# Optimization experiments

Measured on AMD Instinct MI355X. Metric: run time of the kernel, lower is better.

The kernel has to match this reference:

```python
import jax, jax.numpy as jnp
import numpy as np

N_HEAD = 16

def setup_inputs() -> dict:
    key = jax.random.key(0)
    k1, k2, k3 = jax.random.split(key, 3)
    B, T, C = 4, 2048, 1024
    x = jax.random.normal(k1, (B, T, C), dtype=jnp.float32)
    W_attn = jax.random.normal(k2, (C, 3 * C), dtype=jnp.float32) * (1.0 / np.sqrt(C))
    b_attn = jnp.zeros((3 * C,), dtype=jnp.float32)
    W_proj = jax.random.normal(k3, (C, C), dtype=jnp.float32) * (1.0 / np.sqrt(C))
    b_proj = jnp.zeros((C,), dtype=jnp.float32)
    return {"x": x, "W_attn": W_attn, "b_attn": b_attn, "W_proj": W_proj, "b_proj": b_proj, "train": 0}

def reference(x, W_attn, b_attn, W_proj, b_proj, train):
    # Causal self-attention, eval mode (dropout = identity since dropout=0.0 / train=False).
    B, T, C = x.shape
    H = N_HEAD
    hd = C // H
    qkv = x @ W_attn + b_attn                      # [B, T, 3C]
    q, k, v = jnp.split(qkv, 3, axis=-1)
    def to_heads(a):
        return a.reshape(B, T, H, hd).swapaxes(1, 2)   # [B, H, T, hd]
    q, k, v = to_heads(q), to_heads(k), to_heads(v)
    scale = 1.0 / jnp.sqrt(jnp.asarray(hd, dtype=x.dtype))
    attn = jnp.einsum('bhqd,bhkd->bhqk', q, k) * scale   # [B, H, T, T]
    causal = jnp.tril(jnp.ones((T, T), dtype=bool))
    attn = jnp.where(causal, attn, -jnp.inf)
    p = jax.nn.softmax(attn, axis=-1)
    y = jnp.einsum('bhqk,bhkd->bhqd', p, v)              # [B, H, T, hd]
    y = y.swapaxes(1, 2).reshape(B, T, C)
    return y @ W_proj + b_proj
```

## Files before the change

kernel.cpp:

```cpp
#include <hip/hip_runtime.h>
#include <hip/hip_bf16.h>
#include <math.h>

typedef __attribute__((ext_vector_type(8))) short short8;
typedef __attribute__((ext_vector_type(4))) short short4v;
typedef __attribute__((ext_vector_type(4))) float floatx4;
using bf16 = __hip_bfloat16;

#define DEVI __device__ __forceinline__

DEVI floatx4 fzero4() { floatx4 z; z[0]=0.f; z[1]=0.f; z[2]=0.f; z[3]=0.f; return z; }

DEVI float ex2(float x) {
  float r;
  asm("v_exp_f32 %0, %1" : "=v"(r) : "v"(x));
  return r;
}

DEVI unsigned short f2b(float x) {
  union { bf16 h; unsigned short u; } c;
  c.h = __float2bfloat16(x);
  return c.u;
}

DEVI floatx4 mfma16(short4v a, short4v b, floatx4 c) {
#if __has_builtin(__builtin_amdgcn_mfma_f32_16x16x16bf16_1k)
  return __builtin_amdgcn_mfma_f32_16x16x16bf16_1k(a, b, c, 0, 0, 0);
#else
  floatx4 d;
  asm("v_mfma_f32_16x16x16_bf16 %0, %1, %2, %3" : "=v"(d) : "v"(a), "v"(b), "v"(c));
  return d;
#endif
}

DEVI void gload16(const bf16* g, bf16* l) {
  typedef __attribute__((address_space(1))) const void gv_t;
  typedef __attribute__((address_space(3))) void lv_t;
  __builtin_amdgcn_global_load_lds((gv_t*)g, (lv_t*)l, 16, 0, 0);
}

__global__ __launch_bounds__(256) void k_cast(const float* __restrict__ in,
                                              bf16* __restrict__ out, int n) {
  int i = (blockIdx.x * 256 + threadIdx.x) * 8;
  if (i >= n) return;
  float4 a = *(const float4*)(in + i);
  float4 b = *(const float4*)(in + i + 4);
  short8 v;
  v[0] = (short)f2b(a.x); v[1] = (short)f2b(a.y);
  v[2] = (short)f2b(a.z); v[3] = (short)f2b(a.w);
  v[4] = (short)f2b(b.x); v[5] = (short)f2b(b.y);
  v[6] = (short)f2b(b.z); v[7] = (short)f2b(b.w);
  *(short8*)(out + i) = v;
}

__global__ __launch_bounds__(256) void k_transpose(const float* __restrict__ in,
                                                   bf16* __restrict__ out,
                                                   int R, int C) {
  __shared__ float tile[32][33];
  int x = blockIdx.x * 32 + threadIdx.x;
  for (int i = threadIdx.y; i < 32; i += 8) {
    int y = blockIdx.y * 32 + i;
    tile[i][threadIdx.x] = (y < R && x < C) ? in[(size_t)y * C + x] : 0.f;
  }
  __syncthreads();
  int ox = blockIdx.y * 32 + threadIdx.x;
  for (int i = threadIdx.y; i < 32; i += 8) {
    int oy = blockIdx.x * 32 + i;
    if (oy < C && ox < R) out[(size_t)oy * R + ox] = __float2bfloat16(tile[threadIdx.x][i]);
  }
}

template<int MODE>
__global__ __launch_bounds__(256) void k_gemm(
    const bf16* __restrict__ A, const bf16* __restrict__ Bt,
    const float* __restrict__ bias,
    bf16* __restrict__ Qo, bf16* __restrict__ Ko, bf16* __restrict__ Vo,
    float* __restrict__ Fo, int M, int N, int Kd) {
  __shared__ bf16 sA[2][128 * 32];
  __shared__ bf16 sB[2][128 * 32];
  const int tid = threadIdx.x;
  const int w = tid >> 6, l = tid & 63;
  const int lg = l >> 4, li = l & 15;
  const int wr = w >> 1, wc = w & 1;
  const int ii = blockIdx.x >> 3, xcd = blockIdx.x & 7;
  const int bx = ii >> 3, by = xcd * 8 + (ii & 7);
  const int m0 = by * 128, n0 = bx * 128;

  const int r0 = tid >> 2, ko0 = (tid & 3) * 8;
  const bf16* pa0 = A + (size_t)(m0 + r0) * Kd + ko0;
  const bf16* pa1 = A + (size_t)(m0 + 64 + r0) * Kd + ko0;
  const bf16* pb0 = Bt + (size_t)(n0 + r0) * Kd + ko0;
  const bf16* pb1 = Bt + (size_t)(n0 + 64 + r0) * Kd + ko0;

  floatx4 acc[4][4];
#pragma unroll
  for (int i = 0; i < 4; ++i)
#pragma unroll
    for (int j = 0; j < 4; ++j) acc[i][j] = fzero4();

  auto STAGE = [&](int buf, int k0) {
    gload16(pa0 + k0, &sA[buf][w * 512]);
    gload16(pa1 + k0, &sA[buf][2048 + w * 512]);
    gload16(pb0 + k0, &sB[buf][w * 512]);
    gload16(pb1 + k0, &sB[buf][2048 + w * 512]);
  };

  STAGE(0, 0);
  int cur = 0;
  for (int k0 = 0; k0 < Kd; k0 += 32) {
    if (k0 + 32 < Kd) {
      STAGE(cur ^ 1, k0 + 32);
      asm volatile("s_waitcnt vmcnt(4)" ::: "memory");
    } else {
      asm volatile("s_waitcnt vmcnt(0)" ::: "memory");
    }
    __builtin_amdgcn_s_barrier();
    short8 af[4], bfr[4];
#pragma unroll
    for (int i = 0; i < 4; ++i)
      af[i] = *(const short8*)&sA[cur][(wr * 64 + i * 16 + li) * 32 + lg * 8];
#pragma unroll
    for (int j = 0; j < 4; ++j)
      bfr[j] = *(const short8*)&sB[cur][(wc * 64 + j * 16 + li) * 32 + lg * 8];
#pragma unroll
    for (int i = 0; i < 4; ++i)
#pragma unroll
      for (int j = 0; j < 4; ++j)
        acc[i][j] = __builtin_amdgcn_mfma_f32_16x16x32_bf16(af[i], bfr[j], acc[i][j], 0, 0, 0);
    __builtin_amdgcn_s_barrier();
    cur ^= 1;
  }

#pragma unroll
  for (int i = 0; i < 4; ++i) {
#pragma unroll
    for (int j = 0; j < 4; ++j) {
      const int ng = n0 + wc * 64 + j * 16 + li;
      const float bs = bias[ng];
#pragma unroll
      for (int r = 0; r < 4; ++r) {
        const int mg = m0 + wr * 64 + i * 16 + lg * 4 + r;
        const float v = acc[i][j][r] + bs;
        if (MODE == 0) {
          const int bb = mg >> 11, t = mg & 2047;
          const int d = ng & 63;
          if (ng < 1024) {
            const int h = ng >> 6;
            Qo[(((size_t)bb * 16 + h) * 2048 + t) * 64 + d] = __float2bfloat16(v * 0.18033688011112042f);
          } else if (ng < 2048) {
            const int h = (ng - 1024) >> 6;
            Ko[(((size_t)bb * 16 + h) * 2048 + t) * 64 + d] = __float2bfloat16(v);
          } else {
            const int h = (ng - 2048) >> 6;
            Vo[(((size_t)bb * 16 + h) * 64 + d) * 2048 + t] = __float2bfloat16(v);
          }
        } else {
          Fo[(size_t)mg * N + ng] = v;
        }
      }
    }
  }
}

#define T_SEQ 2048

__global__ __launch_bounds__(256) void k_attn(
    const bf16* __restrict__ Q, const bf16* __restrict__ K,
    const bf16* __restrict__ Vt, bf16* __restrict__ Y) {
  __shared__ bf16 sK[2][64 * 64];
  __shared__ bf16 sV[2][64 * 64];

  const int tid = threadIdx.x;
  const int w = tid >> 6, l = tid & 63;
  const int lg = l >> 4, li = l & 15;
  const int bid = blockIdx.x;
  const int s = bid >> 3;
  const int bh = (bid & 7) * 8 + (s & 7);
  const int tb = 15 - (s >> 3);
  const int b = bh >> 4, h = bh & 15;

  const bf16* Qp = Q + (size_t)bh * (T_SEQ * 64);
  const bf16* Kp = K + (size_t)bh * (T_SEQ * 64);
  const bf16* Vp = Vt + (size_t)bh * (64 * T_SEQ);

  const int q0 = tb * 128;
  const int wq0 = q0 + w * 32;
  const int nst = (q0 + 128) >> 6;

  short8 aq[2][2];
#pragma unroll
  for (int rg = 0; rg < 2; ++rg)
#pragma unroll
    for (int dc = 0; dc < 2; ++dc)
      aq[rg][dc] = *(const short8*)(Qp + (size_t)(wq0 + rg * 16 + li) * 64 + dc * 32 + lg * 8);

  floatx4 o[2][4];
#pragma unroll
  for (int rg = 0; rg < 2; ++rg)
#pragma unroll
    for (int f = 0; f < 4; ++f) o[rg][f] = fzero4();
  float m[2] = {-INFINITY, -INFINITY};
  float lsum[2] = {0.f, 0.f};

  auto STAGE = [&](int buf, int k0) {
#pragma unroll
    for (int half = 0; half < 2; ++half) {
      const int c = half * 256 + tid;
      const int row = c >> 3, cs = c & 7;
      const int sc = cs ^ (row & 7);
      bf16* kb = &sK[buf][(half * 256 + w * 64) * 8];
      bf16* vb = &sV[buf][(half * 256 + w * 64) * 8];
      gload16(Kp + (size_t)(k0 + row) * 64 + sc * 8, kb);
      gload16(Vp + (size_t)row * T_SEQ + k0 + sc * 8, vb);
    }
  };

  int cur = 0;
  STAGE(0, 0);
  for (int t = 0; t < nst; ++t) {
    const int k0 = t << 6;
    if (t + 1 < nst) {
      STAGE(cur ^ 1, k0 + 64);
      asm volatile("s_waitcnt vmcnt(4)" ::: "memory");
    } else {
      asm volatile("s_waitcnt vmcnt(0)" ::: "memory");
    }
    __builtin_amdgcn_s_barrier();
    if (k0 <= wq0 + 31) {
      floatx4 s[2][4];
#pragma unroll
      for (int kt = 0; kt < 4; ++kt) {
        const int rowk = kt * 16 + li;
        const short8 kb0 = *(const short8*)&sK[cur][rowk * 64 + ((lg ^ (rowk & 7)) * 8)];
        const short8 kb1 = *(const short8*)&sK[cur][rowk * 64 + (((4 + lg) ^ (rowk & 7)) * 8)];
#pragma unroll
        for (int rg = 0; rg < 2; ++rg) {
          floatx4 acc = __builtin_amdgcn_mfma_f32_16x16x32_bf16(kb0, aq[rg][0], fzero4(), 0, 0, 0);
          s[rg][kt] = __builtin_amdgcn_mfma_f32_16x16x32_bf16(kb1, aq[rg][1], acc, 0, 0, 0);
        }
      }
      if (k0 + 63 > wq0) {
#pragma unroll
        for (int rg = 0; rg < 2; ++rg) {
          const int qg = wq0 + rg * 16 + li;
#pragma unroll
          for (int kt = 0; kt < 4; ++kt) {
            const int kgb = k0 + kt * 16 + lg * 4;
#pragma unroll
            for (int r = 0; r < 4; ++r)
              if (kgb + r > qg) s[rg][kt][r] = -1e30f;
          }
        }
      }
      float pm[2];
#pragma unroll
      for (int rg = 0; rg < 2; ++rg) {
        float m0_ = fmaxf(fmaxf(s[rg][0][0], s[rg][0][1]), fmaxf(s[rg][0][2], s[rg][0][3]));
        float m1_ = fmaxf(fmaxf(s[rg][1][0], s[rg][1][1]), fmaxf(s[rg][1][2], s[rg][1][3]));
        float m2_ = fmaxf(fmaxf(s[rg][2][0], s[rg][2][1]), fmaxf(s[rg][2][2], s[rg][2][3]));
        float m3_ = fmaxf(fmaxf(s[rg][3][0], s[rg][3][1]), fmaxf(s[rg][3][2], s[rg][3][3]));
        float p = fmaxf(fmaxf(m0_, m1_), fmaxf(m2_, m3_));
        p = fmaxf(p, __shfl_xor(p, 16));
        p = fmaxf(p, __shfl_xor(p, 32));
        pm[rg] = p;
      }
      const float need = fmaxf(pm[0] - m[0], pm[1] - m[1]);
      if (!__all(need <= 8.0f)) {
#pragma unroll
        for (int rg = 0; rg < 2; ++rg) {
          const float mn = fmaxf(m[rg], pm[rg]);
          const float a = ex2(m[rg] - mn);
          m[rg] = mn;
          lsum[rg] *= a;
          float ar[4];
#pragma unroll
          for (int r = 0; r < 4; ++r) ar[r] = __shfl(a, lg * 4 + r);
#pragma unroll
          for (int f = 0; f < 4; ++f) {
            o[rg][f][0] *= ar[0]; o[rg][f][1] *= ar[1];
            o[rg][f][2] *= ar[2]; o[rg][f][3] *= ar[3];
          }
        }
      }
      short4v pa4[2][4];
#pragma unroll
      for (int rg = 0; rg < 2; ++rg) {
#pragma unroll
        for (int kt = 0; kt < 4; ++kt) {
          const float e0 = ex2(s[rg][kt][0] - m[rg]);
          const float e1 = ex2(s[rg][kt][1] - m[rg]);
          const float e2 = ex2(s[rg][kt][2] - m[rg]);
          const float e3 = ex2(s[rg][kt][3] - m[rg]);
          lsum[rg] += (e0 + e1) + (e2 + e3);
          short4v pv;
          pv[0] = (short)f2b(e0); pv[1] = (short)f2b(e1);
          pv[2] = (short)f2b(e2); pv[3] = (short)f2b(e3);
          pa4[rg][kt] = pv;
        }
      }
#pragma unroll
      for (int f = 0; f < 4; ++f) {
        const int rowv = f * 16 + li;
        const int rx = rowv & 7;
#pragma unroll
        for (int kt = 0; kt < 4; ++kt) {
          const int cc = 2 * kt + (lg >> 1);
          const short4v vb4 = *(const short4v*)&sV[cur][rowv * 64 + (((cc ^ rx) << 3) | ((lg & 1) << 2))];
          o[0][f] = mfma16(pa4[0][kt], vb4, o[0][f]);
          o[1][f] = mfma16(pa4[1][kt], vb4, o[1][f]);
        }
      }
    }
    __builtin_amdgcn_s_barrier();
    cur ^= 1;
  }
#pragma unroll
  for (int rg = 0; rg < 2; ++rg) {
    float Ls = lsum[rg];
    Ls += __shfl_xor(Ls, 16);
    Ls += __shfl_xor(Ls, 32);
#pragma unroll
    for (int r = 0; r < 4; ++r) {
      const float inv = 1.0f / __shfl(Ls, lg * 4 + r);
      const int qg = wq0 + rg * 16 + lg * 4 + r;
      const size_t base = ((size_t)b * T_SEQ + qg) * 1024 + h * 64;
#pragma unroll
      for (int f = 0; f < 4; ++f)
        Y[base + f * 16 + li] = __float2bfloat16(o[rg][f][r] * inv);
    }
  }
}

extern "C" void kernel_launch(void* const* d_in, const int* in_sizes, int n_in,
                              void* d_out, int out_size, void* d_ws, size_t ws_size,
                              hipStream_t stream) {
  const float* x      = (const float*)d_in[0];
  const float* W_attn = (const float*)d_in[1];
  const float* b_attn = (const float*)d_in[2];
  const float* W_proj = (const float*)d_in[3];
  const float* b_proj = (const float*)d_in[4];
  float* out = (float*)d_out;

  char* ws = (char*)d_ws;
  bf16* Wt_a = (bf16*)(ws);
  bf16* Wt_p = (bf16*)(ws + 6291456);
  bf16* Qb   = (bf16*)(ws + 8388608);
  bf16* Kb   = (bf16*)(ws + 25165824);
  bf16* Vtb  = (bf16*)(ws + 41943040);
  bf16* x_bf = (bf16*)(ws + 58720256);
  bf16* Yb   = x_bf;

  k_cast<<<4096, 256, 0, stream>>>(x, x_bf, 8388608);
  k_transpose<<<dim3(96, 32), dim3(32, 8), 0, stream>>>(W_attn, Wt_a, 1024, 3072);
  k_transpose<<<dim3(32, 32), dim3(32, 8), 0, stream>>>(W_proj, Wt_p, 1024, 1024);
  k_gemm<0><<<1536, 256, 0, stream>>>(x_bf, Wt_a, b_attn, Qb, Kb, Vtb,
                                      nullptr, 8192, 3072, 1024);
  k_attn<<<1024, 256, 0, stream>>>(Qb, Kb, Vtb, Yb);
  k_gemm<1><<<512, 256, 0, stream>>>(Yb, Wt_p, b_proj, nullptr, nullptr,
                                     nullptr, out, 8192, 1024, 1024);
}
```

Baseline: 199.0 us.

## Vectorize V epilogue stores, reorder attention tiles, add setprio and max3

The QKV GEMM epilogue now writes transposed V as packed 4-element bf16 vectors and hoists index math out of the per-row loop. The attention block-to-query-tile mapping is changed to interleave long and short causal tiles across quarters, aiming to balance load across CUs. MFMA sections are wrapped in s_setprio so matrix work gets issue priority over other waves, and the row-max reduction uses v_max3_f32 to cut instruction count. These are several independent micro-optimizations, and the tile reordering may alter cache locality.

```diff
diff --git a/kernel.cpp b/kernel.cpp
--- a/kernel.cpp
+++ b/kernel.cpp
@@ -15,6 +15,12 @@
   float r;
   asm("v_exp_f32 %0, %1" : "=v"(r) : "v"(x));
   return r;
+}
+
+DEVI float max3f(float a, float b, float c) {
+  float d;
+  asm("v_max3_f32 %0, %1, %2, %3" : "=v"(d) : "v"(a), "v"(b), "v"(c));
+  return d;
 }
 
 DEVI unsigned short f2b(float x) {
@@ -137,26 +143,33 @@
     for (int j = 0; j < 4; ++j) {
       const int ng = n0 + wc * 64 + j * 16 + li;
       const float bs = bias[ng];
-#pragma unroll
-      for (int r = 0; r < 4; ++r) {
-        const int mg = m0 + wr * 64 + i * 16 + lg * 4 + r;
-        const float v = acc[i][j][r] + bs;
-        if (MODE == 0) {
-          const int bb = mg >> 11, t = mg & 2047;
-          const int d = ng & 63;
-          if (ng < 1024) {
-            const int h = ng >> 6;
-            Qo[(((size_t)bb * 16 + h) * 2048 + t) * 64 + d] = __float2bfloat16(v * 0.18033688011112042f);
-          } else if (ng < 2048) {
-            const int h = (ng - 1024) >> 6;
-            Ko[(((size_t)bb * 16 + h) * 2048 + t) * 64 + d] = __float2bfloat16(v);
-          } else {
-            const int h = (ng - 2048) >> 6;
-            Vo[(((size_t)bb * 16 + h) * 64 + d) * 2048 + t] = __float2bfloat16(v);
-          }
+      const int mgb = m0 + wr * 64 + i * 16 + lg * 4;
+      if (MODE == 0) {
+        const int bb = mgb >> 11, t = mgb & 2047;
+        const int d = ng & 63;
+        if (ng < 1024) {
+          const int h = ng >> 6;
+#pragma unroll
+          for (int r = 0; r < 4; ++r)
+            Qo[(((size_t)bb * 16 + h) * 2048 + t + r) * 64 + d] =
+                __float2bfloat16((acc[i][j][r] + bs) * 0.18033688011112042f);
+        } else if (ng < 2048) {
+          const int h = (ng - 1024) >> 6;
+#pragma unroll
+          for (int r = 0; r < 4; ++r)
+            Ko[(((size_t)bb * 16 + h) * 2048 + t + r) * 64 + d] =
+                __float2bfloat16(acc[i][j][r] + bs);
         } else {
-          Fo[(size_t)mg * N + ng] = v;
-        }
+          const int h = (ng - 2048) >> 6;
+          short4v vv;
+#pragma unroll
+          for (int r = 0; r < 4; ++r) vv[r] = (short)f2b(acc[i][j][r] + bs);
+          *(short4v*)&Vo[(((size_t)bb * 16 + h) * 64 + d) * 2048 + t] = vv;
+        }
+      } else {
+#pragma unroll
+        for (int r = 0; r < 4; ++r)
+          Fo[(size_t)(mgb + r) * N + ng] = acc[i][j][r] + bs;
       }
     }
   }
@@ -174,9 +187,11 @@
   const int w = tid >> 6, l = tid & 63;
   const int lg = l >> 4, li = l & 15;
   const int bid = blockIdx.x;
-  const int s = bid >> 3;
-  const int bh = (bid & 7) * 8 + (s & 7);
-  const int tb = 15 - (s >> 3);
+  const int sq = bid >> 3;
+  const int bh = (bid & 7) * 8 + (sq & 7);
+  const int g = sq >> 3;
+  const int qd = g >> 2, rr = g & 3;
+  const int tb = (qd == 0) ? 15 - rr : (qd == 1) ? 8 + rr : (qd == 2) ? 7 - rr : rr;
   const int b = bh >> 4, h = bh & 15;
 
   const bf16* Qp = Q + (size_t)bh * (T_SEQ * 64);
@@ -228,6 +243,7 @@
     __builtin_amdgcn_s_barrier();
     if (k0 <= wq0 + 31) {
       floatx4 s[2][4];
+      __builtin_amdgcn_s_setprio(1);
 #pragma unroll
       for (int kt = 0; kt < 4; ++kt) {
         const int rowk = kt * 16 + li;
@@ -239,6 +255,7 @@
           s[rg][kt] = __builtin_amdgcn_mfma_f32_16x16x32_bf16(kb1, aq[rg][1], acc, 0, 0, 0);
         }
       }
+      __builtin_amdgcn_s_setprio(0);
       if (k0 + 63 > wq0) {
 #pragma unroll
         for (int rg = 0; rg < 2; ++rg) {
@@ -255,11 +272,12 @@
       float pm[2];
 #pragma unroll
       for (int rg = 0; rg < 2; ++rg) {
-        float m0_ = fmaxf(fmaxf(s[rg][0][0], s[rg][0][1]), fmaxf(s[rg][0][2], s[rg][0][3]));
-        float m1_ = fmaxf(fmaxf(s[rg][1][0], s[rg][1][1]), fmaxf(s[rg][1][2], s[rg][1][3]));
-        float m2_ = fmaxf(fmaxf(s[rg][2][0], s[rg][2][1]), fmaxf(s[rg][2][2], s[rg][2][3]));
-        float m3_ = fmaxf(fmaxf(s[rg][3][0], s[rg][3][1]), fmaxf(s[rg][3][2], s[rg][3][3]));
-        float p = fmaxf(fmaxf(m0_, m1_), fmaxf(m2_, m3_));
+        float t0 = max3f(s[rg][0][0], s[rg][0][1], s[rg][0][2]);
+        float t1 = max3f(s[rg][0][3], s[rg][1][0], s[rg][1][1]);
+        float t2 = max3f(s[rg][1][2], s[rg][1][3], s[rg][2][0]);
+        float t3 = max3f(s[rg][2][1], s[rg][2][2], s[rg][2][3]);
+        float t4 = max3f(s[rg][3][0], s[rg][3][1], s[rg][3][2]);
+        float p = fmaxf(max3f(t0, t1, t2), max3f(t3, t4, s[rg][3][3]));
         p = fmaxf(p, __shfl_xor(p, 16));
         p = fmaxf(p, __shfl_xor(p, 32));
         pm[rg] = p;
@@ -298,6 +316,7 @@
           pa4[rg][kt] = pv;
         }
       }
+      __builtin_amdgcn_s_setprio(1);
 #pragma unroll
       for (int f = 0; f < 4; ++f) {
         const int rowv = f * 16 + li;
@@ -310,6 +329,7 @@
           o[1][f] = mfma16(pa4[1][kt], vb4, o[1][f]);
         }
       }
+      __builtin_amdgcn_s_setprio(0);
     }
     __builtin_amdgcn_s_barrier();
     cur ^= 1;
```

Result: faster. 189.5 us (-4.8%).
